# Kernel optimization log

Hardware: AMD Instinct MI355X
Metric: run time of the kernel (lower is better)

## Reference

```python
import jax, jax.numpy as jnp
import numpy as np

N, D, E, NNZ = 2048, 4096, 16384, 65536


def setup_inputs() -> dict:
    key = jax.random.key(0)
    k1, k2, k3, k4 = jax.random.split(key, 4)
    x = jax.random.normal(k1, (N, D), dtype=jnp.float32)
    a_values = jax.random.normal(k2, (NNZ,), dtype=jnp.float32)
    a_row_idx = jax.random.randint(k3, (NNZ,), 0, D, dtype=jnp.int32)
    a_col_idx = jax.random.randint(k4, (NNZ,), 0, E, dtype=jnp.int32)
    return {"x": x, "a_values": a_values, "a_row_idx": a_row_idx,
            "a_col_idx": a_col_idx, "num_columns": E}


def reference(x, a_values, a_row_idx, a_col_idx, num_columns):
    # result[n, e] = logsumexp_{k : col[k]==e} ( x[n, row[k]] + vals[k] )
    # terms: (nnz, N) -- one summand per nonzero of A, per row of x
    terms = x.T[a_row_idx] + a_values[:, None]
    # numerically stable segment logsumexp over the column index
    seg_max = jax.ops.segment_max(terms, a_col_idx, num_segments=num_columns)  # (E, N)
    m_safe = jnp.where(jnp.isfinite(seg_max), seg_max, 0.0)                     # empty cols -> 0
    sums = jax.ops.segment_sum(jnp.exp(terms - m_safe[a_col_idx]), a_col_idx,
                               num_segments=num_columns)                        # (E, N)
    result = jnp.log(sums) + m_safe                                             # empty cols -> -inf
    return result.T  # (N, E)
```

## Files before the change

### kernel.cpp

```cpp
#include <hip/hip_runtime.h>
#include <math.h>

#define N   2048
#define D   4096
#define E   16384
#define NNZ 65536

#define CAP  32
#define CAP2 8
#define EC   32
#define NC   256
#define NCP  260

typedef float floatx4 __attribute__((ext_vector_type(4)));
typedef unsigned short ushort_t;

__device__ __forceinline__ ushort_t f2bf(float f) {
    unsigned u = __float_as_uint(f);
    return (ushort_t)((u + 0x7fffu + ((u >> 16) & 1u)) >> 16);
}
__device__ __forceinline__ float bflo(unsigned u) { return __uint_as_float(u << 16); }
__device__ __forceinline__ float bfhi(unsigned u) { return __uint_as_float(u & 0xffff0000u); }

__global__ void fill_kernel(const float* __restrict__ vals, const int* __restrict__ rows,
                            const int* __restrict__ cols, int* __restrict__ counts,
                            int2* __restrict__ pairs) {
    int k = blockIdx.x * blockDim.x + threadIdx.x;
    if (k < NNZ) {
        int c = cols[k];
        int slot = atomicAdd(&counts[c], 1);
        if (slot < CAP)
            pairs[(size_t)c * CAP + slot] = make_int2(rows[k], __float_as_int(__expf(vals[k])));
    }
}

__global__ void expT_kernel(const float* __restrict__ x, ushort_t* __restrict__ xT) {
    __shared__ float tile[32][33];
    int d0 = blockIdx.x * 32, n0 = blockIdx.y * 32;
    int tx = threadIdx.x;
    int ty = threadIdx.y;
    float4 v = *(const float4*)(x + (size_t)(n0 + ty) * D + d0 + tx * 4);
    tile[ty][tx * 4 + 0] = __expf(v.x);
    tile[ty][tx * 4 + 1] = __expf(v.y);
    tile[ty][tx * 4 + 2] = __expf(v.z);
    tile[ty][tx * 4 + 3] = __expf(v.w);
    __syncthreads();
    ushort4 o;
    o.x = f2bf(tile[tx * 4 + 0][ty]);
    o.y = f2bf(tile[tx * 4 + 1][ty]);
    o.z = f2bf(tile[tx * 4 + 2][ty]);
    o.w = f2bf(tile[tx * 4 + 3][ty]);
    *(ushort4*)(xT + (size_t)(d0 + ty) * N + n0 + tx * 4) = o;
}

__global__ __launch_bounds__(256) void lse_kernel(
        const ushort_t* __restrict__ expxT, const int* __restrict__ counts,
        const int2* __restrict__ pairs, float* __restrict__ out) {
    __shared__ char lds_raw[EC * NCP * 4];
    int2* meta = (int2*)lds_raw;
    int*  cnts = (int*)(lds_raw + EC * CAP2 * 8);
    float* res = (float*)lds_raw;

    int bid = blockIdx.x;
    int nb  = bid & 7;
    int cb  = bid >> 3;
    int tid = threadIdx.x;
    int nt  = tid & 63;
    int cg  = __builtin_amdgcn_readfirstlane(tid >> 6);
    int h   = (nt >> 5) & 1;
    int l32 = nt & 31;
    int n0  = nb * NC;
    int n   = n0 + l32 * 8;

    {
        int col = tid >> 3, slot = tid & 7;
        int c = counts[cb * EC + col];
        c = (c > CAP) ? CAP : c;
        int2 pr = pairs[(size_t)(cb * EC + col) * CAP + slot];
        if (slot >= c) pr = make_int2(0, 0);
        meta[col * CAP2 + slot] = pr;
        if (slot == 0) cnts[col] = c;
    }
    __syncthreads();

    float acc[4][8];
    int ebase_l = cg * 8;
#pragma unroll
    for (int p = 0; p < 4; p++) {
        int el = ebase_l + 2 * p + h;
        const int2* mp = meta + el * CAP2;
        float s0=0.f,s1=0.f,s2=0.f,s3=0.f,s4=0.f,s5=0.f,s6=0.f,s7=0.f;
#pragma unroll
        for (int j = 0; j < CAP2; j++) {
            int2 pr = mp[j];
            float ev = __int_as_float(pr.y);
            uint4 xv = *(const uint4*)(expxT + (size_t)pr.x * N + n);
            s0 += bflo(xv.x) * ev; s1 += bfhi(xv.x) * ev;
            s2 += bflo(xv.y) * ev; s3 += bfhi(xv.y) * ev;
            s4 += bflo(xv.z) * ev; s5 += bfhi(xv.z) * ev;
            s6 += bflo(xv.w) * ev; s7 += bfhi(xv.w) * ev;
        }
        int cnt  = cnts[el];
        int cmax = max(cnts[ebase_l + 2 * p], cnts[ebase_l + 2 * p + 1]);
        if (cmax > CAP2) {
            const int2* gp = pairs + (size_t)(cb * EC + el) * CAP;
            for (int j = CAP2; j < cmax; j++) {
                int2 pr = gp[j];
                bool act = j < cnt;
                int   row = act ? pr.x : 0;
                float ev  = act ? __int_as_float(pr.y) : 0.0f;
                uint4 xv = *(const uint4*)(expxT + (size_t)row * N + n);
                s0 += bflo(xv.x) * ev; s1 += bfhi(xv.x) * ev;
                s2 += bflo(xv.y) * ev; s3 += bfhi(xv.y) * ev;
                s4 += bflo(xv.z) * ev; s5 += bfhi(xv.z) * ev;
                s6 += bflo(xv.w) * ev; s7 += bfhi(xv.w) * ev;
            }
        }
        acc[p][0] = cnt ? __logf(s0) : 0.0f;
        acc[p][1] = cnt ? __logf(s1) : 0.0f;
        acc[p][2] = cnt ? __logf(s2) : 0.0f;
        acc[p][3] = cnt ? __logf(s3) : 0.0f;
        acc[p][4] = cnt ? __logf(s4) : 0.0f;
        acc[p][5] = cnt ? __logf(s5) : 0.0f;
        acc[p][6] = cnt ? __logf(s6) : 0.0f;
        acc[p][7] = cnt ? __logf(s7) : 0.0f;
    }
    __syncthreads();

#pragma unroll
    for (int p = 0; p < 4; p++) {
        int el = ebase_l + 2 * p + h;
        *(float4*)(&res[el * NCP + l32 * 8])     =
            make_float4(acc[p][0], acc[p][1], acc[p][2], acc[p][3]);
        *(float4*)(&res[el * NCP + l32 * 8 + 4]) =
            make_float4(acc[p][4], acc[p][5], acc[p][6], acc[p][7]);
    }
    __syncthreads();

    int el4 = (tid & 7) * 4;
    int e_out = cb * EC + el4;
    for (int np = tid >> 3; np < NC; np += 32) {
        floatx4 o;
        o.x = res[(el4 + 0) * NCP + np];
        o.y = res[(el4 + 1) * NCP + np];
        o.z = res[(el4 + 2) * NCP + np];
        o.w = res[(el4 + 3) * NCP + np];
        __builtin_nontemporal_store(o, (floatx4*)(out + (size_t)(n0 + np) * E + e_out));
    }
}

extern "C" void kernel_launch(void* const* d_in, const int* in_sizes, int n_in,
                              void* d_out, int out_size, void* d_ws, size_t ws_size,
                              hipStream_t stream) {
    const float* x      = (const float*)d_in[0];
    const float* a_vals = (const float*)d_in[1];
    const int*   a_rows = (const int*)d_in[2];
    const int*   a_cols = (const int*)d_in[3];
    float* out = (float*)d_out;

    char* ws = (char*)d_ws;
    size_t p = 0;
    auto take = [&](size_t bytes) { size_t cur = p; p += (bytes + 255) & ~(size_t)255; return cur; };
    int*      counts = (int*)(ws + take((size_t)E * 4));
    int2*     pairs  = (int2*)(ws + take((size_t)E * CAP * 8));
    ushort_t* expxT  = (ushort_t*)(ws + take((size_t)D * N * 2));

    (void)hipMemsetAsync(counts, 0, (size_t)E * 4, stream);
    fill_kernel<<<NNZ / 256, 256, 0, stream>>>(a_vals, a_rows, a_cols, counts, pairs);
    expT_kernel<<<dim3(D / 32, N / 32), dim3(8, 32), 0, stream>>>(x, expxT);
    lse_kernel<<<(E / EC) * (N / NC), 256, 0, stream>>>(expxT, counts, pairs, out);
}
```

Before: 204.6 us.

## Switch exp(x) storage to fp16 with packed half2 FMA and halve LDS staging

Stores exp(x) transposed as fp16 instead of bf16 and accumulates the per-column sums with packed __hfma2 in half precision, after first batching all eight gathered row loads before any math. The LDS transpose buffer is halved, with the output written in two passes of 128 rows, to cut shared-memory footprint and allow more resident blocks. Accumulating in fp16 risks overflow or precision loss, since exp values of normal inputs times exp(vals) summed over up to 32 terms can exceed the fp16 range. The two-pass staging also adds extra barriers.

Measured after the change: 200.1 us. -2.2%, faster.

```diff
diff --git a/kernel.cpp b/kernel.cpp
--- a/kernel.cpp
+++ b/kernel.cpp
@@ -1,4 +1,5 @@
 #include <hip/hip_runtime.h>
+#include <hip/hip_fp16.h>
 #include <math.h>
 
 #define N   2048
@@ -10,17 +11,14 @@
 #define CAP2 8
 #define EC   32
 #define NC   256
-#define NCP  260
+#define NCH  133
 
 typedef float floatx4 __attribute__((ext_vector_type(4)));
 typedef unsigned short ushort_t;
 
-__device__ __forceinline__ ushort_t f2bf(float f) {
-    unsigned u = __float_as_uint(f);
-    return (ushort_t)((u + 0x7fffu + ((u >> 16) & 1u)) >> 16);
+__device__ __forceinline__ __half2 u2h2(unsigned u) {
+    union { unsigned u; __half2 h; } c; c.u = u; return c.h;
 }
-__device__ __forceinline__ float bflo(unsigned u) { return __uint_as_float(u << 16); }
-__device__ __forceinline__ float bfhi(unsigned u) { return __uint_as_float(u & 0xffff0000u); }
 
 __global__ void fill_kernel(const float* __restrict__ vals, const int* __restrict__ rows,
                             const int* __restrict__ cols, int* __restrict__ counts,
@@ -46,17 +44,17 @@
     tile[ty][tx * 4 + 3] = __expf(v.w);
     __syncthreads();
     ushort4 o;
-    o.x = f2bf(tile[tx * 4 + 0][ty]);
-    o.y = f2bf(tile[tx * 4 + 1][ty]);
-    o.z = f2bf(tile[tx * 4 + 2][ty]);
-    o.w = f2bf(tile[tx * 4 + 3][ty]);
+    o.x = __half_as_ushort(__float2half_rn(tile[tx * 4 + 0][ty]));
+    o.y = __half_as_ushort(__float2half_rn(tile[tx * 4 + 1][ty]));
+    o.z = __half_as_ushort(__float2half_rn(tile[tx * 4 + 2][ty]));
+    o.w = __half_as_ushort(__float2half_rn(tile[tx * 4 + 3][ty]));
     *(ushort4*)(xT + (size_t)(d0 + ty) * N + n0 + tx * 4) = o;
 }
 
 __global__ __launch_bounds__(256) void lse_kernel(
         const ushort_t* __restrict__ expxT, const int* __restrict__ counts,
         const int2* __restrict__ pairs, float* __restrict__ out) {
-    __shared__ char lds_raw[EC * NCP * 4];
+    __shared__ char lds_raw[EC * NCH * 4];
     int2* meta = (int2*)lds_raw;
     int*  cnts = (int*)(lds_raw + EC * CAP2 * 8);
     float* res = (float*)lds_raw;
@@ -83,22 +81,27 @@
     }
     __syncthreads();
 
-    float acc[4][8];
+    float facc[4][8];
     int ebase_l = cg * 8;
 #pragma unroll
     for (int p = 0; p < 4; p++) {
         int el = ebase_l + 2 * p + h;
         const int2* mp = meta + el * CAP2;
-        float s0=0.f,s1=0.f,s2=0.f,s3=0.f,s4=0.f,s5=0.f,s6=0.f,s7=0.f;
+        uint4  xv[CAP2];
+        __half2 ev2[CAP2];
 #pragma unroll
         for (int j = 0; j < CAP2; j++) {
             int2 pr = mp[j];
-            float ev = __int_as_float(pr.y);
-            uint4 xv = *(const uint4*)(expxT + (size_t)pr.x * N + n);
-            s0 += bflo(xv.x) * ev; s1 += bfhi(xv.x) * ev;
-            s2 += bflo(xv.y) * ev; s3 += bfhi(xv.y) * ev;
-            s4 += bflo(xv.z) * ev; s5 += bfhi(xv.z) * ev;
-            s6 += bflo(xv.w) * ev; s7 += bfhi(xv.w) * ev;
+            ev2[j] = __float2half2_rn(__int_as_float(pr.y));
+            xv[j]  = *(const uint4*)(expxT + (size_t)pr.x * N + n);
+        }
+        __half2 a0 = __float2half2_rn(0.f), a1 = a0, a2 = a0, a3 = a0;
+#pragma unroll
+        for (int j = 0; j < CAP2; j++) {
+            a0 = __hfma2(u2h2(xv[j].x), ev2[j], a0);
+            a1 = __hfma2(u2h2(xv[j].y), ev2[j], a1);
+            a2 = __hfma2(u2h2(xv[j].z), ev2[j], a2);
+            a3 = __hfma2(u2h2(xv[j].w), ev2[j], a3);
         }
         int cnt  = cnts[el];
         int cmax = max(cnts[ebase_l + 2 * p], cnts[ebase_l + 2 * p + 1]);
@@ -108,44 +111,50 @@
                 int2 pr = gp[j];
                 bool act = j < cnt;
                 int   row = act ? pr.x : 0;
-                float ev  = act ? __int_as_float(pr.y) : 0.0f;
-                uint4 xv = *(const uint4*)(expxT + (size_t)row * N + n);
-                s0 += bflo(xv.x) * ev; s1 += bfhi(xv.x) * ev;
-                s2 += bflo(xv.y) * ev; s3 += bfhi(xv.y) * ev;
-                s4 += bflo(xv.z) * ev; s5 += bfhi(xv.z) * ev;
-                s6 += bflo(xv.w) * ev; s7 += bfhi(xv.w) * ev;
+                __half2 e2 = __float2half2_rn(act ? __int_as_float(pr.y) : 0.0f);
+                uint4 x2 = *(const uint4*)(expxT + (size_t)row * N + n);
+                a0 = __hfma2(u2h2(x2.x), e2, a0);
+                a1 = __hfma2(u2h2(x2.y), e2, a1);
+                a2 = __hfma2(u2h2(x2.z), e2, a2);
+                a3 = __hfma2(u2h2(x2.w), e2, a3);
             }
         }
-        acc[p][0] = cnt ? __logf(s0) : 0.0f;
-        acc[p][1] = cnt ? __logf(s1) : 0.0f;
-        acc[p][2] = cnt ? __logf(s2) : 0.0f;
-        acc[p][3] = cnt ? __logf(s3) : 0.0f;
-        acc[p][4] = cnt ? __logf(s4) : 0.0f;
-        acc[p][5] = cnt ? __logf(s5) : 0.0f;
-        acc[p][6] = cnt ? __logf(s6) : 0.0f;
-        acc[p][7] = cnt ? __logf(s7) : 0.0f;
+        facc[p][0] = cnt ? __logf(__low2float(a0))  : 0.0f;
+        facc[p][1] = cnt ? __logf(__high2float(a0)) : 0.0f;
+        facc[p][2] = cnt ? __logf(__low2float(a1))  : 0.0f;
+        facc[p][3] = cnt ? __logf(__high2float(a1)) : 0.0f;
+        facc[p][4] = cnt ? __logf(__low2float(a2))  : 0.0f;
+        facc[p][5] = cnt ? __logf(__high2float(a2)) : 0.0f;
+        facc[p][6] = cnt ? __logf(__low2float(a3))  : 0.0f;
+        facc[p][7] = cnt ? __logf(__high2float(a3)) : 0.0f;
     }
-    __syncthreads();
-
-#pragma unroll
-    for (int p = 0; p < 4; p++) {
-        int el = ebase_l + 2 * p + h;
-        *(float4*)(&res[el * NCP + l32 * 8])     =
-            make_float4(acc[p][0], acc[p][1], acc[p][2], acc[p][3]);
-        *(float4*)(&res[el * NCP + l32 * 8 + 4]) =
-            make_float4(acc[p][4], acc[p][5], acc[p][6], acc[p][7]);
-    }
-    __syncthreads();
 
     int el4 = (tid & 7) * 4;
     int e_out = cb * EC + el4;
-    for (int np = tid >> 3; np < NC; np += 32) {
-        floatx4 o;
-        o.x = res[(el4 + 0) * NCP + np];
-        o.y = res[(el4 + 1) * NCP + np];
-        o.z = res[(el4 + 2) * NCP + np];
-        o.w = res[(el4 + 3) * NCP + np];
-        __builtin_nontemporal_store(o, (floatx4*)(out + (size_t)(n0 + np) * E + e_out));
+#pragma unroll
+    for (int half = 0; half < 2; half++) {
+        __syncthreads();
+        if ((l32 >> 4) == half) {
+            int nl = (l32 & 15) * 8;
+#pragma unroll
+            for (int p = 0; p < 4; p++) {
+                int el = ebase_l + 2 * p + h;
+                *(float4*)(&res[el * NCH + nl]) =
+                    make_float4(facc[p][0], facc[p][1], facc[p][2], facc[p][3]);
+                *(float4*)(&res[el * NCH + nl + 4]) =
+                    make_float4(facc[p][4], facc[p][5], facc[p][6], facc[p][7]);
+            }
+        }
+        __syncthreads();
+        for (int np = tid >> 3; np < 128; np += 32) {
+            floatx4 o;
+            o.x = res[(el4 + 0) * NCH + np];
+            o.y = res[(el4 + 1) * NCH + np];
+            o.z = res[(el4 + 2) * NCH + np];
+            o.w = res[(el4 + 3) * NCH + np];
+            __builtin_nontemporal_store(
+                o, (floatx4*)(out + (size_t)(n0 + half * 128 + np) * E + e_out));
+        }
     }
 }
 
```
